# Kernel optimization log

Hardware: AMD Instinct MI355X
Metric: run time of the kernel (lower is better)

Reference implementation:

```python
import jax, jax.numpy as jnp
import numpy as np
from jax import lax

# 4D convolution via lax.conv_general_dilated (supports N spatial dims natively)
# Layout: x is (N, C, T, U, V, W); weight is (O, I, kT, kU, kV, kW)

def conv4d(x, w, b):
    dn = lax.conv_dimension_numbers(x.shape, w.shape, ('NCTUVW', 'OITUVW', 'NCTUVW'))
    y = lax.conv_general_dilated(x, w, window_strides=(1, 1, 1, 1), padding='SAME',
                                 dimension_numbers=dn)
    return y + b[None, :, None, None, None, None]


def setup_inputs() -> dict:
    key = jax.random.key(0)
    k0, k1, k2, k3, k4 = jax.random.split(key, 5)
    B, C_in, C_hid, C_out = 2, 64, 128, 64
    T, D, H, W = 4, 16, 32, 32
    K = 3  # kernel size per dim (stmode 'C' -> (3,3,3,3))
    x = jax.random.normal(k0, (B, C_in, T, D, H, W), dtype=jnp.float32)
    scale1 = 1.0 / np.sqrt(C_in * K ** 4)
    scale2 = 1.0 / np.sqrt(C_hid * K ** 4)
    w1 = jax.random.normal(k1, (C_hid, C_in, K, K, K, K), dtype=jnp.float32) * scale1
    b1 = jax.random.normal(k2, (C_hid,), dtype=jnp.float32) * scale1
    w2 = jax.random.normal(k3, (C_out, C_hid, K, K, K, K), dtype=jnp.float32) * scale2
    b2 = jax.random.normal(k4, (C_out,), dtype=jnp.float32) * scale2
    return {"x": x, "w1": w1, "b1": b1, "w2": w2, "b2": b2}


def reference(x, w1, b1, w2, b2):
    # conv1 -> ReLU -> (dropout p=0 is identity) -> conv2 -> (dropout identity)
    h = jax.nn.relu(conv4d(x, w1, b1))
    return conv4d(h, w2, b2)
```

## Files before the change

kernel.cpp:

```cpp
#include <hip/hip_runtime.h>


using bf16x8 = __attribute__((ext_vector_type(8))) __bf16;
using f32x16 = __attribute__((ext_vector_type(16))) float;
using f32x4  = __attribute__((ext_vector_type(4))) float;

typedef __attribute__((address_space(1))) const void as1_void;
typedef __attribute__((address_space(3))) void as3_void;
__device__ __forceinline__ void gload_lds16(const void* g, void* l) {
    __builtin_amdgcn_global_load_lds((as1_void*)g, (as3_void*)l, 16, 0, 0);
}

__global__ __launch_bounds__(256) void cvt_x(const float* __restrict__ x,
                                             __bf16* __restrict__ x_t) {
    __shared__ float lt[64][65];
    const int nb = blockIdx.y;
    const int p0 = blockIdx.x * 64;
    const float* src = x + (size_t)nb * 64 * 65536;
    __bf16* dst = x_t + (size_t)nb * 65536 * 64;
    #pragma unroll
    for (int i = 0; i < 16; ++i) {
        int idx = i * 256 + threadIdx.x;
        int c = idx >> 6, p = idx & 63;
        lt[c][p] = src[(size_t)c * 65536 + p0 + p];
    }
    __syncthreads();
    #pragma unroll
    for (int i = 0; i < 16; ++i) {
        int idx = i * 256 + threadIdx.x;
        int p = idx >> 6, c = idx & 63;
        dst[(size_t)(p0 + p) * 64 + c] = (__bf16)lt[c][p];
    }
}

template <int CIN>
__global__ __launch_bounds__(256) void cvt_w(const float* __restrict__ w,
                                             __bf16* __restrict__ wt) {
    constexpr int LOG = (CIN == 64) ? 6 : 7;
    constexpr int COUT = 8192 / CIN;
    int oc = blockIdx.x * 256 + threadIdx.x;
    if (oc >= 8192) return;
    const int o = oc >> LOG, c = oc & (CIN - 1);
    const int kg = c >> 4, cl = c & 15;
    const float* src = w + (size_t)oc * 81;
    #pragma unroll 1
    for (int tap = 0; tap < 81; ++tap)
        wt[(((size_t)tap * (CIN / 16) + kg) * COUT + o) * 16 + cl] = (__bf16)src[tap];
}

template <int CIN, int COUT, int NT, bool RELU>
__global__ __launch_bounds__(256, 2) void conv4d_mfma(
    const __bf16* __restrict__ in_t,
    const __bf16* __restrict__ wt,
    const float* __restrict__ bias,
    __bf16* __restrict__ out_bf,
    float* __restrict__ out_f,
    const __bf16* __restrict__ zp)
{
    constexpr int KST   = CIN / 16;
    constexpr int UNITS = CIN / 32;
    constexpr int LOGU  = (UNITS == 2) ? 1 : 2;
    __shared__ __bf16 tile[2 * 12288];

    const int tid  = threadIdx.x;
    const int lane = tid & 63;
    const int l31  = lane & 31;
    const int hl   = lane >> 5;
    const int wv   = tid >> 6;
    const int gmi  = wv >> 1;
    const int gni  = wv & 1;

    const int bid = blockIdx.x;
    const int xcd = bid & 7;
    const int s0  = bid >> 3;
    const int u   = xcd * 2 + (s0 & 1);
    const int vg  = (s0 >> 1) & 3;
    const int t   = (s0 >> 3) & 3;
    const int nb  = (s0 >> 5) & 1;
    const int v0  = vg * 8;
    const int pbase = ((t * 16 + u) * 32 + v0) * 32;

    const __bf16* inb = in_t + (size_t)nb * 65536 * CIN;

    int goff[6];
    #pragma unroll
    for (int r = 0; r < 6; ++r) {
        const int slot = r * 256 + tid;
        const int row  = slot / 136;
        const int rem  = slot - row * 136;
        const int chunk = rem / 34;
        const int wp   = rem - chunk * 34;
        const int v_in = v0 - 1 + row;
        const int w_in = wp - 1;
        const bool ok = (row < 10) && ((unsigned)v_in < 32u) && ((unsigned)w_in < 32u);
        goff[r] = ok ? ((v_in * 32 + w_in) * CIN + chunk * 8) : -1;
    }

    const int lane_base = (gmi * 16 + hl) * 34 + l31;
    const bf16x8* tile16 = (const bf16x8*)tile;

    const __bf16* wlane[NT];
    #pragma unroll
    for (int nt = 0; nt < NT; ++nt)
        wlane[nt] = wt + ((gni * NT + nt) * 32 + l31) * 16 + hl * 8;

    int sb[9], tb0[9], nst = 0;
    #pragma unroll
    for (int kt = 0; kt < 3; ++kt) {
        const int t_in = t + kt - 1;
        if ((unsigned)t_in >= 4u) continue;
        #pragma unroll
        for (int ku = 0; ku < 3; ++ku) {
            const int u_in = u + ku - 1;
            if ((unsigned)u_in >= 16u) continue;
            sb[nst]  = (t_in * 16 + u_in) * 1024 * CIN;
            tb0[nst] = (kt * 3 + ku) * 9;
            ++nst;
        }
    }
    const int U = nst * UNITS;

    f32x16 acc[4][NT];
    #pragma unroll
    for (int mt = 0; mt < 4; ++mt)
        #pragma unroll
        for (int nt = 0; nt < NT; ++nt)
            #pragma unroll
            for (int i = 0; i < 16; ++i)
                acc[mt][nt][i] = 0.f;

    auto issue = [&](int j) {
        const int st = j >> LOGU, ch = j & (UNITS - 1);
        const __bf16* gb = inb + sb[st] + ch * 32;
        char* lb = ((char*)tile) + (j & 1) * 24576 + wv * 1024;
        #pragma unroll
        for (int r = 0; r < 6; ++r) {
            const __bf16* gp = (goff[r] >= 0) ? (gb + goff[r]) : zp;
            gload_lds16(gp, lb + r * 4096);
        }
    };

    issue(0);
    #pragma unroll 1
    for (int i = 0; i < U; ++i) {
        __syncthreads();
        if (i + 1 < U) issue(i + 1);

        const int st = i >> LOGU, ch = i & (UNITS - 1);
        const int tapb = tb0[st];
        const bf16x8* tb = tile16 + (i & 1) * 1536 + lane_base;
        #pragma unroll
        for (int ks = 0; ks < 2; ++ks) {
            const int ksg = ch * 2 + ks;
            #pragma unroll
            for (int kw = 0; kw < 3; ++kw) {
                bf16x8 af[6];
                #pragma unroll
                for (int r = 0; r < 6; ++r)
                    af[r] = tb[kw + 34 * (4 * r + 2 * ks)];
                bf16x8 bv[3][NT];
                #pragma unroll
                for (int kv = 0; kv < 3; ++kv) {
                    const size_t wo =
                        ((size_t)(tapb + kv * 3 + kw) * KST + ksg) * (COUT * 16);
                    #pragma unroll
                    for (int nt = 0; nt < NT; ++nt)
                        bv[kv][nt] = *(const bf16x8*)(wlane[nt] + wo);
                }
                #pragma unroll
                for (int kv = 0; kv < 3; ++kv)
                    #pragma unroll
                    for (int rr = 0; rr < 4; ++rr)
                        #pragma unroll
                        for (int nt = 0; nt < NT; ++nt)
                            acc[rr][nt] = __builtin_amdgcn_mfma_f32_32x32x16_bf16(
                                af[kv + rr], bv[kv][nt], acc[rr][nt], 0, 0, 0);
            }
        }
    }

    #pragma unroll
    for (int nt = 0; nt < NT; ++nt) {
        const int o = (gni * NT + nt) * 32 + l31;
        const float bvls = bias[o];
        #pragma unroll
        for (int mt = 0; mt < 4; ++mt) {
            const int pb = pbase + (gmi * 4 + mt) * 32;
            if constexpr (RELU) {
                #pragma unroll
                for (int rg = 0; rg < 4; ++rg)
                    #pragma unroll
                    for (int j = 0; j < 4; ++j) {
                        float v = acc[mt][nt][rg * 4 + j] + bvls;
                        v = v > 0.f ? v : 0.f;
                        const int p = pb + j + 8 * rg + 4 * hl;
                        out_bf[(size_t)(nb * 65536 + p) * COUT + o] = (__bf16)v;
                    }
            } else {
                #pragma unroll
                for (int rg = 0; rg < 4; ++rg) {
                    f32x4 sv;
                    #pragma unroll
                    for (int j = 0; j < 4; ++j)
                        sv[j] = acc[mt][nt][rg * 4 + j] + bvls;
                    const int p = pb + 8 * rg + 4 * hl;
                    *(f32x4*)(out_f + ((size_t)nb * COUT + o) * 65536 + p) = sv;
                }
            }
        }
    }
}

extern "C" void kernel_launch(void* const* d_in, const int* in_sizes, int n_in,
                              void* d_out, int out_size, void* d_ws, size_t ws_size,
                              hipStream_t stream) {
    const float* x  = (const float*)d_in[0];
    const float* w1 = (const float*)d_in[1];
    const float* b1 = (const float*)d_in[2];
    const float* w2 = (const float*)d_in[3];
    const float* b2 = (const float*)d_in[4];
    float* out = (float*)d_out;

    char* ws = (char*)d_ws;
    __bf16* x_t = (__bf16*)ws;
    __bf16* h_t = (__bf16*)(ws + 16777216);
    __bf16* w1t = (__bf16*)(ws + 50331648);
    __bf16* w2t = (__bf16*)(ws + 51658752);
    __bf16* zp  = (__bf16*)(ws + 52985856);

    hipMemsetAsync(zp, 0, 256, stream);
    cvt_x<<<dim3(1024, 2), 256, 0, stream>>>(x, x_t);
    cvt_w<64><<<32, 256, 0, stream>>>(w1, w1t);
    cvt_w<128><<<32, 256, 0, stream>>>(w2, w2t);

    conv4d_mfma<64, 128, 2, true><<<512, 256, 0, stream>>>(x_t, w1t, b1, h_t,
                                                           nullptr, zp);
    conv4d_mfma<128, 64, 1, false><<<512, 256, 0, stream>>>(h_t, w2t, b2, nullptr,
                                                            out, zp);
}
```

Measured before the change: 415.6 us.

## Halve conv spatial tile, reorder activations channel-chunked, and raise occupancy

Changes the intermediate activation layout to (t,u,v) rows split into 8-channel chunks that are contiguous along w, so each 16-byte global-to-LDS load reads consecutive w positions. Halves the per-block spatial tile from 8 to 4 v-rows, which shrinks LDS and accumulator use. The grid doubles to 1024 blocks and launch bounds allow 3 or 4 blocks per CU. Padding is zeroed once in LDS instead of loading from a zero page, and an explicit vmcnt wait is added before each barrier. The cost is a larger halo overhead, since 6 input rows feed 4 output rows instead of 10 feeding 8, and weight loads are amortised over fewer outputs.

```diff
diff --git a/kernel.cpp b/kernel.cpp
--- a/kernel.cpp
+++ b/kernel.cpp
@@ -16,6 +16,7 @@
     __shared__ float lt[64][65];
     const int nb = blockIdx.y;
     const int p0 = blockIdx.x * 64;
+    const int tu = p0 >> 10;
     const float* src = x + (size_t)nb * 64 * 65536;
     __bf16* dst = x_t + (size_t)nb * 65536 * 64;
     #pragma unroll
@@ -28,8 +29,11 @@
     #pragma unroll
     for (int i = 0; i < 16; ++i) {
         int idx = i * 256 + threadIdx.x;
-        int p = idx >> 6, c = idx & 63;
-        dst[(size_t)(p0 + p) * 64 + c] = (__bf16)lt[c][p];
+        int c = idx >> 6, pl = idx & 63;
+        int p = p0 + pl;
+        int v = (p >> 5) & 31, w = p & 31;
+        dst[(size_t)(tu * 32 + v) * 2048 + (c >> 3) * 256 + w * 8 + (c & 7)] =
+            (__bf16)lt[c][pl];
     }
 }
 
@@ -48,19 +52,18 @@
         wt[(((size_t)tap * (CIN / 16) + kg) * COUT + o) * 16 + cl] = (__bf16)src[tap];
 }
 
-template <int CIN, int COUT, int NT, bool RELU>
-__global__ __launch_bounds__(256, 2) void conv4d_mfma(
+template <int CIN, int COUT, int NT, int WPEU, bool RELU>
+__global__ __launch_bounds__(256, WPEU) void conv4d_mfma(
     const __bf16* __restrict__ in_t,
     const __bf16* __restrict__ wt,
     const float* __restrict__ bias,
     __bf16* __restrict__ out_bf,
-    float* __restrict__ out_f,
-    const __bf16* __restrict__ zp)
+    float* __restrict__ out_f)
 {
     constexpr int KST   = CIN / 16;
     constexpr int UNITS = CIN / 32;
     constexpr int LOGU  = (UNITS == 2) ? 1 : 2;
-    __shared__ __bf16 tile[2 * 12288];
+    __shared__ __bf16 tile[2 * 6528];
 
     const int tid  = threadIdx.x;
     const int lane = tid & 63;
@@ -74,17 +77,17 @@
     const int xcd = bid & 7;
     const int s0  = bid >> 3;
     const int u   = xcd * 2 + (s0 & 1);
-    const int vg  = (s0 >> 1) & 3;
-    const int t   = (s0 >> 3) & 3;
-    const int nb  = (s0 >> 5) & 1;
-    const int v0  = vg * 8;
+    const int vg  = (s0 >> 1) & 7;
+    const int t   = (s0 >> 4) & 3;
+    const int nb  = (s0 >> 6) & 1;
+    const int v0  = vg * 4;
     const int pbase = ((t * 16 + u) * 32 + v0) * 32;
 
     const __bf16* inb = in_t + (size_t)nb * 65536 * CIN;
 
-    int goff[6];
-    #pragma unroll
-    for (int r = 0; r < 6; ++r) {
+    int goff[4];
+    #pragma unroll
+    for (int r = 0; r < 4; ++r) {
         const int slot = r * 256 + tid;
         const int row  = slot / 136;
         const int rem  = slot - row * 136;
@@ -92,11 +95,20 @@
         const int wp   = rem - chunk * 34;
         const int v_in = v0 - 1 + row;
         const int w_in = wp - 1;
-        const bool ok = (row < 10) && ((unsigned)v_in < 32u) && ((unsigned)w_in < 32u);
-        goff[r] = ok ? ((v_in * 32 + w_in) * CIN + chunk * 8) : -1;
-    }
-
-    const int lane_base = (gmi * 16 + hl) * 34 + l31;
+        const bool ok = (row < 6) && ((unsigned)v_in < 32u) && ((unsigned)w_in < 32u);
+        goff[r] = ok ? (v_in * (CIN * 32) + chunk * 256 + w_in * 8) : -1;
+    }
+
+    #pragma unroll
+    for (int r = 0; r < 4; ++r) {
+        const int slot = r * 256 + tid;
+        if (slot < 816 && goff[r] < 0) {
+            *(uint4*)((char*)tile + slot * 16) = make_uint4(0u, 0u, 0u, 0u);
+            *(uint4*)((char*)tile + 13056 + slot * 16) = make_uint4(0u, 0u, 0u, 0u);
+        }
+    }
+
+    const int lane_base = gmi * 2 * 136 + hl * 34 + l31;
     const bf16x8* tile16 = (const bf16x8*)tile;
 
     const __bf16* wlane[NT];
@@ -120,9 +132,9 @@
     }
     const int U = nst * UNITS;
 
-    f32x16 acc[4][NT];
-    #pragma unroll
-    for (int mt = 0; mt < 4; ++mt)
+    f32x16 acc[2][NT];
+    #pragma unroll
+    for (int mt = 0; mt < 2; ++mt)
         #pragma unroll
         for (int nt = 0; nt < NT; ++nt)
             #pragma unroll
@@ -131,33 +143,33 @@
 
     auto issue = [&](int j) {
         const int st = j >> LOGU, ch = j & (UNITS - 1);
-        const __bf16* gb = inb + sb[st] + ch * 32;
-        char* lb = ((char*)tile) + (j & 1) * 24576 + wv * 1024;
-        #pragma unroll
-        for (int r = 0; r < 6; ++r) {
-            const __bf16* gp = (goff[r] >= 0) ? (gb + goff[r]) : zp;
-            gload_lds16(gp, lb + r * 4096);
-        }
+        const __bf16* gb = inb + sb[st] + ch * 1024;
+        char* lb = ((char*)tile) + (j & 1) * 13056 + wv * 1024;
+        #pragma unroll
+        for (int r = 0; r < 4; ++r)
+            if (goff[r] >= 0)
+                gload_lds16(gb + goff[r], lb + r * 4096);
     };
 
     issue(0);
     #pragma unroll 1
     for (int i = 0; i < U; ++i) {
+        asm volatile("s_waitcnt vmcnt(0) lgkmcnt(0)" ::: "memory");
         __syncthreads();
         if (i + 1 < U) issue(i + 1);
 
         const int st = i >> LOGU, ch = i & (UNITS - 1);
         const int tapb = tb0[st];
-        const bf16x8* tb = tile16 + (i & 1) * 1536 + lane_base;
+        const bf16x8* tb = tile16 + (i & 1) * 816 + lane_base;
         #pragma unroll
         for (int ks = 0; ks < 2; ++ks) {
             const int ksg = ch * 2 + ks;
             #pragma unroll
             for (int kw = 0; kw < 3; ++kw) {
-                bf16x8 af[6];
-                #pragma unroll
-                for (int r = 0; r < 6; ++r)
-                    af[r] = tb[kw + 34 * (4 * r + 2 * ks)];
+                bf16x8 af[4];
+                #pragma unroll
+                for (int r = 0; r < 4; ++r)
+                    af[r] = tb[r * 136 + ks * 68 + kw];
                 bf16x8 bv[3][NT];
                 #pragma unroll
                 for (int kv = 0; kv < 3; ++kv) {
@@ -170,11 +182,11 @@
                 #pragma unroll
                 for (int kv = 0; kv < 3; ++kv)
                     #pragma unroll
-                    for (int rr = 0; rr < 4; ++rr)
+                    for (int rr = 0; rr < 2; ++rr)
                         #pragma unroll
                         for (int nt = 0; nt < NT; ++nt)
                             acc[rr][nt] = __builtin_amdgcn_mfma_f32_32x32x16_bf16(
-                                af[kv + rr], bv[kv][nt], acc[rr][nt], 0, 0, 0);
+                                af[rr + kv], bv[kv][nt], acc[rr][nt], 0, 0, 0);
             }
         }
     }
@@ -184,8 +196,8 @@
         const int o = (gni * NT + nt) * 32 + l31;
         const float bvls = bias[o];
         #pragma unroll
-        for (int mt = 0; mt < 4; ++mt) {
-            const int pb = pbase + (gmi * 4 + mt) * 32;
+        for (int mt = 0; mt < 2; ++mt) {
+            const int pb = pbase + (gmi * 2 + mt) * 32;
             if constexpr (RELU) {
                 #pragma unroll
                 for (int rg = 0; rg < 4; ++rg)
@@ -194,7 +206,10 @@
                         float v = acc[mt][nt][rg * 4 + j] + bvls;
                         v = v > 0.f ? v : 0.f;
                         const int p = pb + j + 8 * rg + 4 * hl;
-                        out_bf[(size_t)(nb * 65536 + p) * COUT + o] = (__bf16)v;
+                        const int vv = (p >> 5) & 31, ww = p & 31, tu = p >> 10;
+                        out_bf[(size_t)nb * 65536 * COUT +
+                               (size_t)(tu * 32 + vv) * (32 * COUT) +
+                               (o >> 3) * 256 + ww * 8 + (o & 7)] = (__bf16)v;
                     }
             } else {
                 #pragma unroll
@@ -226,15 +241,13 @@
     __bf16* h_t = (__bf16*)(ws + 16777216);
     __bf16* w1t = (__bf16*)(ws + 50331648);
     __bf16* w2t = (__bf16*)(ws + 51658752);
-    __bf16* zp  = (__bf16*)(ws + 52985856);
-
-    hipMemsetAsync(zp, 0, 256, stream);
+
     cvt_x<<<dim3(1024, 2), 256, 0, stream>>>(x, x_t);
     cvt_w<64><<<32, 256, 0, stream>>>(w1, w1t);
     cvt_w<128><<<32, 256, 0, stream>>>(w2, w2t);
 
-    conv4d_mfma<64, 128, 2, true><<<512, 256, 0, stream>>>(x_t, w1t, b1, h_t,
-                                                           nullptr, zp);
-    conv4d_mfma<128, 64, 1, false><<<512, 256, 0, stream>>>(h_t, w2t, b2, nullptr,
-                                                            out, zp);
-}
+    conv4d_mfma<64, 128, 2, 3, true><<<1024, 256, 0, stream>>>(x_t, w1t, b1, h_t,
+                                                               nullptr);
+    conv4d_mfma<128, 64, 1, 4, false><<<1024, 256, 0, stream>>>(h_t, w2t, b2, nullptr,
+                                                                out);
+}
```

After: 397.8 us. 1.04x faster.
